# Kernel tuning notes

Hardware: AMD Instinct MI355X
Metric: run time of the kernel (lower is better)

Reference implementation:

```python
import jax, jax.numpy as jnp
import numpy as np

N = 4_000_000
TAU = 1.0
LOSS_WEIGHT = 1.0
EPS = 1e-6


def _xy_wh_r_2_xy_sigma_components(xywhr):
    """Convert [N,5] (x,y,w,h,r) boxes to mu [N,2] and 2x2 sigma components.

    sigma = R diag((w/2)^2, (h/2)^2) R^T, returned as (s11, s12, s22) [N] each.
    """
    xy = xywhr[..., :2]
    wh = jnp.clip(xywhr[..., 2:4], 1e-7, 1e7)
    r = xywhr[..., 4]
    c, s = jnp.cos(r), jnp.sin(r)
    a = (0.5 * wh[..., 0]) ** 2  # (w/2)^2
    b = (0.5 * wh[..., 1]) ** 2  # (h/2)^2
    s11 = a * c * c + b * s * s
    s12 = (a - b) * s * c
    s22 = a * s * s + b * c * c
    return xy, s11, s12, s22


def setup_inputs() -> dict:
    key = jax.random.key(0)
    k1, k2 = jax.random.split(key)

    def rand_boxes(k):
        kx, kw, kr = jax.random.split(k, 3)
        xy = jax.random.normal(kx, (N, 2), dtype=jnp.float32) * 10.0
        wh = jax.random.uniform(kw, (N, 2), minval=2.0, maxval=50.0, dtype=jnp.float32)
        r = jax.random.uniform(kr, (N, 1), minval=-np.pi, maxval=np.pi, dtype=jnp.float32)
        return jnp.concatenate([xy, wh, r], axis=-1)

    pred = rand_boxes(k1)
    target = rand_boxes(k2)
    weight = jnp.ones((N,), dtype=jnp.float32)  # all > 0 -> mask keeps all boxes
    return {"pred": pred, "target": target, "weight": weight}


def reference(pred, target, weight):
    # mask = weight > 0 is all-True for weight=ones, so pred[mask] == pred.
    mu_p, p11, p12, p22 = _xy_wh_r_2_xy_sigma_components(pred)
    mu_t, t11, t12, t22 = _xy_wh_r_2_xy_sigma_components(target)

    det_p = p11 * p22 - p12 * p12
    det_t = t11 * t22 - t12 * t12

    dx = mu_p[..., 0] - mu_t[..., 0]
    dy = mu_p[..., 1] - mu_t[..., 1]

    # delta^T Sigma_t^{-1} delta (closed-form 2x2 inverse)
    term1 = (t22 * dx * dx - 2.0 * t12 * dx * dy + t11 * dy * dy) / det_t
    # trace(Sigma_t^{-1} Sigma_p) + log(det Sigma_t / det Sigma_p)
    trace_term = (t22 * p11 - 2.0 * t12 * p12 + t11 * p22) / det_t
    term2 = trace_term + jnp.log(det_t / det_p)

    dis = term1 + term2 - 2.0
    kl_dis = jnp.clip(dis, EPS)
    # fun='sqrt'
    loss = 1.0 - 1.0 / (TAU + jnp.sqrt(kl_dis))
    return loss[:, None] * LOSS_WEIGHT  # [N,1] matching torch keepdim layout
```

## Files before the change

kernel.cpp:

```cpp
#include <hip/hip_runtime.h>
#include <hip/hip_bf16.h>
#include <math.h>

#define EPS 1e-6f
#define TAU 1.0f

typedef float v4f __attribute__((ext_vector_type(4)));

__device__ __forceinline__ float gd_loss_one(
        float px, float py, float pw, float ph, float pr,
        float tx, float ty, float tw, float th, float tr) {
    pw = fminf(fmaxf(pw, 1e-7f), 1e7f);
    ph = fminf(fmaxf(ph, 1e-7f), 1e7f);
    float pa = 0.25f * pw * pw;
    float pb = 0.25f * ph * ph;
    float ps, pc;
    __sincosf(pr, &ps, &pc);
    float p11 = pa * pc * pc + pb * ps * ps;
    float p12 = (pa - pb) * ps * pc;
    float p22 = pa * ps * ps + pb * pc * pc;

    tw = fminf(fmaxf(tw, 1e-7f), 1e7f);
    th = fminf(fmaxf(th, 1e-7f), 1e7f);
    float ta = 0.25f * tw * tw;
    float tb = 0.25f * th * th;
    float ts, tc;
    __sincosf(tr, &ts, &tc);
    float t11 = ta * tc * tc + tb * ts * ts;
    float t12 = (ta - tb) * ts * tc;
    float t22 = ta * ts * ts + tb * tc * tc;

    float det_p = p11 * p22 - p12 * p12;
    float det_t = t11 * t22 - t12 * t12;

    float dx = px - tx;
    float dy = py - ty;

    float inv_det_t = __frcp_rn(det_t);
    float term1 = (t22 * dx * dx - 2.0f * t12 * dx * dy + t11 * dy * dy) * inv_det_t;
    float trace_term = (t22 * p11 - 2.0f * t12 * p12 + t11 * p22) * inv_det_t;
    float term2 = trace_term + __logf(det_t) - __logf(det_p);

    float dis = term1 + term2 - 2.0f;
    float kl = fmaxf(dis, EPS);
    return 1.0f - 1.0f / (TAU + sqrtf(kl));
}

__global__ void __launch_bounds__(256, 8) gd_loss_kernel_nt(
        const v4f* __restrict__ pred4,
        const v4f* __restrict__ tgt4,
        v4f* __restrict__ out4, int nq) {
    int i = blockIdx.x * blockDim.x + threadIdx.x;
    if (i >= nq) return;

    v4f pv[5], tv[5];
    #pragma unroll
    for (int k = 0; k < 5; k++)
        pv[k] = __builtin_nontemporal_load(&pred4[(size_t)i * 5 + k]);
    #pragma unroll
    for (int k = 0; k < 5; k++)
        tv[k] = __builtin_nontemporal_load(&tgt4[(size_t)i * 5 + k]);

    float pf[20], tf[20];
    #pragma unroll
    for (int k = 0; k < 5; k++) {
        #pragma unroll
        for (int j = 0; j < 4; j++) {
            pf[4 * k + j] = pv[k][j];
            tf[4 * k + j] = tv[k][j];
        }
    }

    v4f res;
    #pragma unroll
    for (int b = 0; b < 4; b++) {
        res[b] = gd_loss_one(pf[b * 5 + 0], pf[b * 5 + 1], pf[b * 5 + 2], pf[b * 5 + 3], pf[b * 5 + 4],
                             tf[b * 5 + 0], tf[b * 5 + 1], tf[b * 5 + 2], tf[b * 5 + 3], tf[b * 5 + 4]);
    }
    __builtin_nontemporal_store(res, &out4[i]);
}

__global__ void gd_loss_tail(
        const float* __restrict__ pred,
        const float* __restrict__ tgt,
        float* __restrict__ out, int start, int n) {
    int i = start + blockIdx.x * blockDim.x + threadIdx.x;
    if (i >= n) return;
    const float* p = pred + (size_t)i * 5;
    const float* t = tgt + (size_t)i * 5;
    out[i] = gd_loss_one(p[0], p[1], p[2], p[3], p[4],
                         t[0], t[1], t[2], t[3], t[4]);
}

extern "C" void kernel_launch(void* const* d_in, const int* in_sizes, int n_in,
                              void* d_out, int out_size, void* d_ws, size_t ws_size,
                              hipStream_t stream) {
    const float* pred = (const float*)d_in[0];
    const float* tgt  = (const float*)d_in[1];
    float* out = (float*)d_out;
    int n = out_size;

    int nq = n / 4;
    int rem = n - nq * 4;

    if (nq > 0) {
        int block = 256;
        int grid = (nq + block - 1) / block;
        gd_loss_kernel_nt<<<grid, block, 0, stream>>>(
            (const v4f*)pred, (const v4f*)tgt, (v4f*)out, nq);
    }
    if (rem > 0) {
        gd_loss_tail<<<1, 64, 0, stream>>>(pred, tgt, out, nq * 4, n);
    }
}
```

Baseline: 214.1 us.

## Stage input tiles through LDS for fully coalesced global loads

The kernel now has each block load its contiguous span of pred and target with consecutive threads reading consecutive 16-byte vectors. The data is staged in shared memory, and each thread then reads its own 5-vector record from LDS. This replaces the earlier strided per-thread loads, where each thread fetched 80 contiguous bytes. It also drops the nontemporal load and store hints and the occupancy hint, and adds 40 KB of LDS per block plus a barrier. The LDS use may limit occupancy, and the stride-5 LDS reads may cause bank conflicts.

```diff
diff --git a/kernel.cpp b/kernel.cpp
--- a/kernel.cpp
+++ b/kernel.cpp
@@ -46,20 +46,40 @@
     return 1.0f - 1.0f / (TAU + sqrtf(kl));
 }
 
-__global__ void __launch_bounds__(256, 8) gd_loss_kernel_nt(
+__global__ void __launch_bounds__(256) gd_loss_lds(
         const v4f* __restrict__ pred4,
         const v4f* __restrict__ tgt4,
         v4f* __restrict__ out4, int nq) {
-    int i = blockIdx.x * blockDim.x + threadIdx.x;
-    if (i >= nq) return;
+    __shared__ float p_lds[5120];
+    __shared__ float t_lds[5120];
+
+    int tid = threadIdx.x;
+    size_t tile = blockIdx.x;
+    size_t f4base = tile * 1280;
+    size_t nf4 = (size_t)nq * 5;
+
+    v4f* pl4 = (v4f*)p_lds;
+    v4f* tl4 = (v4f*)t_lds;
+
+    #pragma unroll
+    for (int k = 0; k < 5; k++) {
+        size_t idx = f4base + k * 256 + tid;
+        if (idx < nf4) {
+            pl4[k * 256 + tid] = pred4[idx];
+            tl4[k * 256 + tid] = tgt4[idx];
+        }
+    }
+    __syncthreads();
+
+    size_t q = tile * 256 + tid;
+    if (q >= (size_t)nq) return;
 
     v4f pv[5], tv[5];
     #pragma unroll
-    for (int k = 0; k < 5; k++)
-        pv[k] = __builtin_nontemporal_load(&pred4[(size_t)i * 5 + k]);
-    #pragma unroll
-    for (int k = 0; k < 5; k++)
-        tv[k] = __builtin_nontemporal_load(&tgt4[(size_t)i * 5 + k]);
+    for (int k = 0; k < 5; k++) {
+        pv[k] = pl4[tid * 5 + k];
+        tv[k] = tl4[tid * 5 + k];
+    }
 
     float pf[20], tf[20];
     #pragma unroll
@@ -77,7 +97,7 @@
         res[b] = gd_loss_one(pf[b * 5 + 0], pf[b * 5 + 1], pf[b * 5 + 2], pf[b * 5 + 3], pf[b * 5 + 4],
                              tf[b * 5 + 0], tf[b * 5 + 1], tf[b * 5 + 2], tf[b * 5 + 3], tf[b * 5 + 4]);
     }
-    __builtin_nontemporal_store(res, &out4[i]);
+    out4[q] = res;
 }
 
 __global__ void gd_loss_tail(
@@ -104,9 +124,8 @@
     int rem = n - nq * 4;
 
     if (nq > 0) {
-        int block = 256;
-        int grid = (nq + block - 1) / block;
-        gd_loss_kernel_nt<<<grid, block, 0, stream>>>(
+        int grid = (nq + 255) / 256;
+        gd_loss_lds<<<grid, 256, 0, stream>>>(
             (const v4f*)pred, (const v4f*)tgt, (v4f*)out, nq);
     }
     if (rem > 0) {
```

Measured after the change: 187.3 us. 12.5% less time.

## Use grid-stride loop with register double-buffered prefetch of next quad

Applied to the files above, without the earlier changes.

Replaces the one-quad-per-thread kernel with a persistent grid-stride kernel of at most 1024 blocks. Each thread prefetches the next iteration's 40 input floats into registers while it computes the current quad, so load latency overlaps with math. It also drops the nontemporal load/store builtins and the occupancy hint in launch_bounds. The cost is higher register pressure from the doubled buffers, likely lower occupancy, and fewer waves for a bandwidth-bound kernel.

```diff
diff --git a/kernel.cpp b/kernel.cpp
--- a/kernel.cpp
+++ b/kernel.cpp
@@ -46,21 +46,7 @@
     return 1.0f - 1.0f / (TAU + sqrtf(kl));
 }
 
-__global__ void __launch_bounds__(256, 8) gd_loss_kernel_nt(
-        const v4f* __restrict__ pred4,
-        const v4f* __restrict__ tgt4,
-        v4f* __restrict__ out4, int nq) {
-    int i = blockIdx.x * blockDim.x + threadIdx.x;
-    if (i >= nq) return;
-
-    v4f pv[5], tv[5];
-    #pragma unroll
-    for (int k = 0; k < 5; k++)
-        pv[k] = __builtin_nontemporal_load(&pred4[(size_t)i * 5 + k]);
-    #pragma unroll
-    for (int k = 0; k < 5; k++)
-        tv[k] = __builtin_nontemporal_load(&tgt4[(size_t)i * 5 + k]);
-
+__device__ __forceinline__ v4f gd_loss_quad(const v4f* pv, const v4f* tv) {
     float pf[20], tf[20];
     #pragma unroll
     for (int k = 0; k < 5; k++) {
@@ -70,14 +56,50 @@
             tf[4 * k + j] = tv[k][j];
         }
     }
-
     v4f res;
     #pragma unroll
     for (int b = 0; b < 4; b++) {
         res[b] = gd_loss_one(pf[b * 5 + 0], pf[b * 5 + 1], pf[b * 5 + 2], pf[b * 5 + 3], pf[b * 5 + 4],
                              tf[b * 5 + 0], tf[b * 5 + 1], tf[b * 5 + 2], tf[b * 5 + 3], tf[b * 5 + 4]);
     }
-    __builtin_nontemporal_store(res, &out4[i]);
+    return res;
+}
+
+__global__ void __launch_bounds__(256) gd_loss_pipe(
+        const v4f* __restrict__ pred4,
+        const v4f* __restrict__ tgt4,
+        v4f* __restrict__ out4, int nq) {
+    int stride = gridDim.x * blockDim.x;
+    int i = blockIdx.x * blockDim.x + threadIdx.x;
+    if (i >= nq) return;
+
+    v4f pc[5], tc[5];
+    #pragma unroll
+    for (int k = 0; k < 5; k++) {
+        pc[k] = pred4[(size_t)i * 5 + k];
+        tc[k] = tgt4[(size_t)i * 5 + k];
+    }
+
+    for (;;) {
+        int nx = i + stride;
+        bool has = nx < nq;
+
+        v4f pn[5], tn[5];
+        if (has) {
+            #pragma unroll
+            for (int k = 0; k < 5; k++) {
+                pn[k] = pred4[(size_t)nx * 5 + k];
+                tn[k] = tgt4[(size_t)nx * 5 + k];
+            }
+        }
+
+        out4[i] = gd_loss_quad(pc, tc);
+
+        if (!has) break;
+        #pragma unroll
+        for (int k = 0; k < 5; k++) { pc[k] = pn[k]; tc[k] = tn[k]; }
+        i = nx;
+    }
 }
 
 __global__ void gd_loss_tail(
@@ -105,8 +127,10 @@
 
     if (nq > 0) {
         int block = 256;
-        int grid = (nq + block - 1) / block;
-        gd_loss_kernel_nt<<<grid, block, 0, stream>>>(
+        int grid = 1024;
+        int max_grid = (nq + block - 1) / block;
+        if (grid > max_grid) grid = max_grid;
+        gd_loss_pipe<<<grid, block, 0, stream>>>(
             (const v4f*)pred, (const v4f*)tgt, (v4f*)out, nq);
     }
     if (rem > 0) {
```

Measured after the change: 189.8 us. 11.4% less time.
